# Optimization experiments

Measured on AMD Instinct MI355X. Metric: run time of the kernel, lower is better.

Reference implementation:

```python
import jax, jax.numpy as jnp
import numpy as np

N_HEAD = 16
N_KV_HEAD = 4
N_EMBD = 2048
HEAD_DIM = N_EMBD // N_HEAD
RMS_EPS = float(np.finfo(np.float32).eps)  # torch F.rms_norm default eps


def setup_inputs() -> dict:
    key = jax.random.key(0)
    ks = jax.random.split(key, 7)
    B, T = 2, 2048
    s = 0.02
    return {
        "x": jax.random.normal(ks[0], (B, T, N_EMBD), jnp.float32),
        "cos": jax.random.uniform(ks[1], (T, 1, HEAD_DIM), jnp.float32),
        "sin": jax.random.uniform(ks[2], (T, 1, HEAD_DIM), jnp.float32),
        "wq": jax.random.normal(ks[3], (N_HEAD * HEAD_DIM, N_EMBD), jnp.float32) * s,
        "wk": jax.random.normal(ks[4], (N_KV_HEAD * HEAD_DIM, N_EMBD), jnp.float32) * s,
        "wv": jax.random.normal(ks[5], (N_KV_HEAD * HEAD_DIM, N_EMBD), jnp.float32) * s,
        "wproj": jax.random.normal(ks[6], (N_EMBD, N_EMBD), jnp.float32) * s,
    }


def _rotate_half(x):
    h = x.shape[-1] // 2
    return jnp.concatenate([-x[..., h:], x[..., :h]], axis=-1)


def _apply_rope(x, cos, sin):  # x: [B, T, H, D]; cos/sin: [T, 1, D]
    return x * cos + _rotate_half(x) * sin


def _rms_norm(x):
    var = jnp.mean(jnp.square(x), axis=-1, keepdims=True)
    return x * jax.lax.rsqrt(var + RMS_EPS)


def reference(x, cos, sin, wq, wk, wv, wproj):
    B, T, C = x.shape
    group = N_HEAD // N_KV_HEAD
    q = (x @ wq.T).reshape(B, T, N_HEAD, HEAD_DIM)
    k = (x @ wk.T).reshape(B, T, N_KV_HEAD, HEAD_DIM)
    v = (x @ wv.T).reshape(B, T, N_KV_HEAD, HEAD_DIM)
    q = _rms_norm(_apply_rope(q, cos, sin))  # RoPE then QK RMSNorm
    k = _rms_norm(_apply_rope(k, cos, sin))
    # to [B, H, T, D]; expand kv heads for GQA
    q = q.transpose(0, 2, 1, 3)
    k = jnp.repeat(k.transpose(0, 2, 1, 3), group, axis=1)
    v = jnp.repeat(v.transpose(0, 2, 1, 3), group, axis=1)
    scale = 1.0 / jnp.sqrt(jnp.asarray(HEAD_DIM, x.dtype))
    scores = jnp.einsum('bhqd,bhkd->bhqk', q, k) * scale
    causal = jnp.tril(jnp.ones((T, T), bool))
    scores = jnp.where(causal, scores, jnp.asarray(-jnp.inf, scores.dtype))
    attn = jax.nn.softmax(scores, axis=-1)
    y = jnp.einsum('bhqk,bhkd->bhqd', attn, v)
    y = y.transpose(0, 2, 1, 3).reshape(B, T, C)
    return y @ wproj.T
```

## Files before the change

### kernel.cpp

```cpp
#include <hip/hip_runtime.h>
#include <hip/hip_bf16.h>

typedef __hip_bfloat16 bf16;
typedef __attribute__((ext_vector_type(8))) __bf16 bf16x8;
typedef __attribute__((ext_vector_type(4))) float f32x4;

#define MFMA16(a, b, c) __builtin_amdgcn_mfma_f32_16x16x32_bf16((a), (b), (c), 0, 0, 0)

#define BT 4096
#define CE 2048
#define NQKV 3072
#define TSEQ 2048
#define HD 128

#define QSCALE (0.08838834764831845f * 1.4426950408889634f)
#define M2 16.3222f

__device__ __forceinline__ void gld16(const void* g, void* l)
{
    __builtin_amdgcn_global_load_lds(
        (const __attribute__((address_space(1))) void*)g,
        (__attribute__((address_space(3))) void*)l, 16, 0, 0);
}

__global__ void detect_dtype(const unsigned short* __restrict__ x, int* __restrict__ flag)
{
    __shared__ int cnt;
    if (threadIdx.x == 0) cnt = 0;
    __syncthreads();
    unsigned short w = x[2 * threadIdx.x];
    int e = (w >> 7) & 0xFF;
    atomicAdd(&cnt, (e >= 117 && e <= 130) ? 1 : 0);
    __syncthreads();
    if (threadIdx.x == 0) *flag = (cnt < 128) ? 1 : 0;
}

__device__ __forceinline__ void stage8(short* dst, const void* src, size_t eoff, bool f32)
{
    if (f32) {
        const float* s = (const float*)src + eoff;
        float4 f0 = *(const float4*)s;
        float4 f1 = *(const float4*)(s + 4);
        bf16x8 v;
        v[0] = (__bf16)f0.x; v[1] = (__bf16)f0.y; v[2] = (__bf16)f0.z; v[3] = (__bf16)f0.w;
        v[4] = (__bf16)f1.x; v[5] = (__bf16)f1.y; v[6] = (__bf16)f1.z; v[7] = (__bf16)f1.w;
        *(bf16x8*)dst = v;
    } else {
        *(uint4*)dst = *(const uint4*)((const bf16*)src + eoff);
    }
}

__device__ __forceinline__ float ldf(const void* p, int i, bool f32)
{
    return f32 ? ((const float*)p)[i] : __bfloat162float(((const bf16*)p)[i]);
}

__global__ __launch_bounds__(256)
void conv_bf16(const void* __restrict__ src, bf16* __restrict__ dst,
               const int* __restrict__ flagp)
{
    const bool f = *flagp != 0;
    size_t i8 = (size_t)blockIdx.x * 256 + threadIdx.x;
    stage8((short*)(dst + i8 * 8), src, i8 * 8, f);
}

__global__ __launch_bounds__(256)
void gemm_bt(const void* __restrict__ A, const bf16* __restrict__ W,
             void* __restrict__ C, int M, int N, int K, int lda,
             int aGate, int oGate, const int* __restrict__ flagp)
{
    __shared__ short As[128][32];
    __shared__ short Bs[128][32];

    const int f = *flagp;
    const bool aF = aGate && f, oF = oGate && f;

    const int tid   = threadIdx.x;
    const int lane  = tid & 63;
    const int wid   = tid >> 6;
    const int row16 = lane & 15;
    const int quad  = lane >> 4;
    const int wr    = wid >> 1;
    const int wc    = wid & 1;
    const int m0    = blockIdx.y * 128;
    const int n0    = blockIdx.x * 128;

    const int rl4 = wid * 16 + (lane >> 2);
    const int c8  = (lane & 3) * 8;

    f32x4 acc[4][4];
#pragma unroll
    for (int i = 0; i < 4; i++)
#pragma unroll
        for (int j = 0; j < 4; j++)
            acc[i][j] = (f32x4){0.f, 0.f, 0.f, 0.f};

    for (int k0 = 0; k0 < K; k0 += 32) {
#pragma unroll
        for (int i = 0; i < 2; i++) {
            int r = i * 64 + rl4;
            gld16(W + (size_t)(n0 + r) * K + k0 + c8, &Bs[r][c8]);
        }
        if (!aF) {
#pragma unroll
            for (int i = 0; i < 2; i++) {
                int r = i * 64 + rl4;
                gld16((const bf16*)A + (size_t)(m0 + r) * lda + k0 + c8, &As[r][c8]);
            }
        } else {
#pragma unroll
            for (int i = 0; i < 2; i++) {
                int c = i * 256 + tid;
                int row = c >> 2, col = (c & 3) << 3;
                stage8(&As[row][col], A, (size_t)(m0 + row) * lda + k0 + col, true);
            }
        }
        __syncthreads();

        bf16x8 af[4], bfv[4];
#pragma unroll
        for (int mi = 0; mi < 4; mi++)
            af[mi] = *(const bf16x8*)&As[wr * 64 + mi * 16 + row16][quad * 8];
#pragma unroll
        for (int ni = 0; ni < 4; ni++)
            bfv[ni] = *(const bf16x8*)&Bs[wc * 64 + ni * 16 + row16][quad * 8];
#pragma unroll
        for (int mi = 0; mi < 4; mi++)
#pragma unroll
            for (int ni = 0; ni < 4; ni++)
                acc[mi][ni] = MFMA16(af[mi], bfv[ni], acc[mi][ni]);
        __syncthreads();
    }

#pragma unroll
    for (int mi = 0; mi < 4; mi++) {
        int rowb = m0 + wr * 64 + mi * 16 + quad * 4;
#pragma unroll
        for (int ni = 0; ni < 4; ni++) {
            int col = n0 + wc * 64 + ni * 16 + row16;
#pragma unroll
            for (int r = 0; r < 4; r++) {
                size_t idx = (size_t)(rowb + r) * N + col;
                float  v   = acc[mi][ni][r];
                if (oF) ((float*)C)[idx] = v;
                else    ((bf16*)C)[idx]  = __float2bfloat16(v);
            }
        }
    }
}

__global__ __launch_bounds__(256)
void rope_rms(bf16* __restrict__ qkv, const void* __restrict__ cosp,
              const void* __restrict__ sinp, const int* __restrict__ flagp)
{
    const bool f = *flagp != 0;
    const int wg   = blockIdx.x * 4 + (threadIdx.x >> 6);
    const int lane = threadIdx.x & 63;
    const int s    = wg % 20;
    const int m    = wg / 20;
    const int t    = m & (TSEQ - 1);

    const int col = (s < 16) ? s * HD : CE + (s - 16) * HD;
    bf16* p = qkv + (size_t)m * NQKV + col;

    float xlo = __bfloat162float(p[lane]);
    float xhi = __bfloat162float(p[lane + 64]);
    float cl  = ldf(cosp, t * HD + lane, f);
    float sl  = ldf(sinp, t * HD + lane, f);
    float ch  = ldf(cosp, t * HD + 64 + lane, f);
    float sh  = ldf(sinp, t * HD + 64 + lane, f);

    float rlo = xlo * cl - xhi * sl;
    float rhi = xhi * ch + xlo * sh;

    float ss = rlo * rlo + rhi * rhi;
#pragma unroll
    for (int off = 32; off > 0; off >>= 1)
        ss += __shfl_xor(ss, off, 64);
    float inv = rsqrtf(ss * (1.0f / 128.0f) + 1.1920929e-07f);
    if (s < 16) inv *= QSCALE;

    p[lane]      = __float2bfloat16(rlo * inv);
    p[lane + 64] = __float2bfloat16(rhi * inv);
}

__global__ __launch_bounds__(256)
void vtrans(const bf16* __restrict__ qkv, bf16* __restrict__ vt)
{
    int idx = blockIdx.x * 256 + threadIdx.x;
    int t  = idx & (TSEQ - 1);
    int d  = (idx >> 11) & 127;
    int bh = idx >> 18;
    vt[idx] = qkv[((size_t)((bh >> 2) * TSEQ + t)) * NQKV + 2560 + (bh & 3) * HD + d];
}

__global__ __launch_bounds__(512, 2)
void attn(bf16* __restrict__ qkv, const bf16* __restrict__ vt)
{
    __shared__ __bf16 Ks[2][64][128];
    __shared__ __bf16 Vs[2][128][64];
    __shared__ __bf16 Pl[8][2][16][72];

    const int tid   = threadIdx.x;
    const int lane  = tid & 63;
    const int wid   = tid >> 6;
    const int row16 = lane & 15;
    const int quad  = lane >> 4;
    const int b   = blockIdx.y >> 2;
    const int hk  = blockIdx.y & 3;
    const int h   = hk * 4 + (wid & 3);
    const int mh  = wid >> 2;
    const int xi  = blockIdx.x;
    const int q0  = xi * 64;
    const int qr0 = q0 + mh * 32;

    const bf16* Q  = qkv + ((size_t)(b * TSEQ + qr0)) * NQKV + h * HD;
    const bf16* Kp = qkv + ((size_t)(b * TSEQ)) * NQKV + CE + hk * HD;
    const bf16* Vp = vt + ((size_t)(b * 4 + hk) * HD) * TSEQ;

    char* const KsB = (char*)Ks;
    char* const VsB = (char*)Vs;

    auto stage = [&](int buf, int k0) {
#pragma unroll
        for (int i = 0; i < 2; i++) {
            int kr = (wid << 3) + i * 4 + (lane >> 4);
            int kc = (lane & 15) ^ (kr & 7);
            gld16(Kp + (size_t)(k0 + kr) * NQKV + kc * 8,
                  KsB + buf * 16384 + ((wid << 3) + i * 4) * 256 + lane * 16);
            int vr = (wid << 4) + i * 8 + (lane >> 3);
            int vc = (lane & 7) ^ (vr & 7);
            gld16(Vp + (size_t)vr * TSEQ + k0 + vc * 8,
                  VsB + buf * 16384 + ((wid << 4) + i * 8) * 128 + lane * 16);
        }
    };

    bf16x8 aq[2][4];
#pragma unroll
    for (int mi = 0; mi < 2; mi++)
#pragma unroll
        for (int ds = 0; ds < 4; ds++)
            aq[mi][ds] = *(const bf16x8*)(Q + (size_t)(mi * 16 + row16) * NQKV
                                          + ds * 32 + quad * 8);

    f32x4 o[2][8];
#pragma unroll
    for (int mi = 0; mi < 2; mi++)
#pragma unroll
        for (int dt = 0; dt < 8; dt++)
            o[mi][dt] = (f32x4){0.f, 0.f, 0.f, 0.f};
    float lsum[2][4] = {{0.f, 0.f, 0.f, 0.f}, {0.f, 0.f, 0.f, 0.f}};

    stage(0, 0);
    __syncthreads();

    for (int t = 0; t <= xi; t++) {
        const int cur = t & 1;
        if (t < xi) stage(cur ^ 1, (t + 1) * 64);

        f32x4 s[2][4];
#pragma unroll
        for (int mi = 0; mi < 2; mi++)
#pragma unroll
            for (int kg = 0; kg < 4; kg++)
                s[mi][kg] = (f32x4){0.f, 0.f, 0.f, 0.f};

        __builtin_amdgcn_s_setprio(1);
#pragma unroll
        for (int ds = 0; ds < 4; ds++) {
#pragma unroll
            for (int kg = 0; kg < 4; kg++) {
                int krow = kg * 16 + row16;
                int phys = (ds * 4 + quad) ^ (row16 & 7);
                bf16x8 kf = *(const bf16x8*)(KsB + cur * 16384 + krow * 256 + phys * 16);
                s[0][kg] = MFMA16(aq[0][ds], kf, s[0][kg]);
                s[1][kg] = MFMA16(aq[1][ds], kf, s[1][kg]);
            }
        }
        __builtin_amdgcn_s_setprio(0);

        const bool diag = (t == xi);
        const int  k0   = t * 64;
#pragma unroll
        for (int mi = 0; mi < 2; mi++) {
#pragma unroll
            for (int r = 0; r < 4; r++) {
                float p[4];
                int qrow = qr0 + mi * 16 + quad * 4 + r;
#pragma unroll
                for (int kg = 0; kg < 4; kg++) {
                    float e = __builtin_amdgcn_exp2f(s[mi][kg][r] - M2);
                    p[kg] = (!diag || (k0 + kg * 16 + row16 <= qrow)) ? e : 0.f;
                }
                lsum[mi][r] += (p[0] + p[1]) + (p[2] + p[3]);
#pragma unroll
                for (int kg = 0; kg < 4; kg++)
                    Pl[wid][mi][quad * 4 + r][kg * 16 + row16] = (__bf16)p[kg];
            }
        }
        __asm__ volatile("" ::: "memory");

        __builtin_amdgcn_s_setprio(1);
#pragma unroll
        for (int c = 0; c < 2; c++) {
            bf16x8 pf0 = *(const bf16x8*)&Pl[wid][0][row16][c * 32 + quad * 8];
            bf16x8 pf1 = *(const bf16x8*)&Pl[wid][1][row16][c * 32 + quad * 8];
#pragma unroll
            for (int dt = 0; dt < 8; dt++) {
                int vrow = dt * 16 + row16;
                int phys = (c * 4 + quad) ^ (row16 & 7);
                bf16x8 vf = *(const bf16x8*)(VsB + cur * 16384 + vrow * 128 + phys * 16);
                o[0][dt] = MFMA16(pf0, vf, o[0][dt]);
                o[1][dt] = MFMA16(pf1, vf, o[1][dt]);
            }
        }
        __builtin_amdgcn_s_setprio(0);
        __asm__ volatile("" ::: "memory");
        __syncthreads();
    }

#pragma unroll
    for (int mi = 0; mi < 2; mi++) {
#pragma unroll
        for (int r = 0; r < 4; r++) {
            float l = lsum[mi][r];
#pragma unroll
            for (int off = 1; off < 16; off <<= 1)
                l += __shfl_xor(l, off, 64);
            float rl = 1.0f / l;
            int trow = qr0 + mi * 16 + quad * 4 + r;
            bf16* dst = qkv + ((size_t)(b * TSEQ + trow)) * NQKV + h * HD;
#pragma unroll
            for (int dt = 0; dt < 8; dt++)
                dst[dt * 16 + row16] = __float2bfloat16(o[mi][dt][r] * rl);
        }
    }
}

extern "C" void kernel_launch(void* const* d_in, const int* in_sizes, int n_in,
                              void* d_out, int out_size, void* d_ws, size_t ws_size,
                              hipStream_t stream)
{
    bf16* qkv   = (bf16*)d_ws;
    bf16* vt    = qkv + (size_t)BT * NQKV;
    bf16* wqkvb = vt + (size_t)2 * 4 * HD * TSEQ;
    int* flagp  = (int*)(wqkvb + (size_t)NQKV * CE);

    detect_dtype<<<1, 256, 0, stream>>>((const unsigned short*)d_in[0], flagp);

    conv_bf16<<<(2048 * 2048 / 8) / 256, 256, 0, stream>>>(d_in[3], wqkvb, flagp);
    conv_bf16<<<(512 * 2048 / 8) / 256, 256, 0, stream>>>(d_in[4], wqkvb + (size_t)2048 * 2048, flagp);
    conv_bf16<<<(512 * 2048 / 8) / 256, 256, 0, stream>>>(d_in[5], wqkvb + (size_t)2560 * 2048, flagp);

    gemm_bt<<<dim3(NQKV / 128, BT / 128), 256, 0, stream>>>(
        d_in[0], wqkvb, qkv, BT, NQKV, CE, CE, 1, 0, flagp);

    conv_bf16<<<(2048 * 2048 / 8) / 256, 256, 0, stream>>>(d_in[6], wqkvb, flagp);

    vtrans<<<(2 * 4 * HD * TSEQ) / 256, 256, 0, stream>>>(qkv, vt);

    rope_rms<<<(BT * 20) / 4, 256, 0, stream>>>(qkv, d_in[1], d_in[2], flagp);

    attn<<<dim3(TSEQ / 64, 2 * 4), 512, 0, stream>>>(qkv, vt);

    gemm_bt<<<dim3(CE / 128, BT / 128), 256, 0, stream>>>(
        qkv, wqkvb, d_out, BT, CE, CE, NQKV, 0, 1, flagp);
}
```

Before: 369.1 us.

## Add 256x256 triple-buffered GEMM kernel for QKV and output projections

Adds a new 8-wave GEMM kernel with 256x256 tiles, a three-stage LDS ring fed by direct global-to-LDS loads, XOR swizzling and split MFMA phases with priority hints. The QKV projection now first converts x to bf16 in workspace (when the workspace is large enough) so the new kernel can read it, and the output projection always uses the new kernel. Larger tiles are meant to raise data reuse and overlap loads with MFMA work. The cost is an extra conversion pass over x, and the bigger tiles give only 128 or 192 workgroups, which may underfill the device's compute units.

```diff
diff --git a/kernel.cpp b/kernel.cpp
--- a/kernel.cpp
+++ b/kernel.cpp
@@ -135,6 +135,131 @@
 #pragma unroll
     for (int mi = 0; mi < 4; mi++) {
         int rowb = m0 + wr * 64 + mi * 16 + quad * 4;
+#pragma unroll
+        for (int ni = 0; ni < 4; ni++) {
+            int col = n0 + wc * 64 + ni * 16 + row16;
+#pragma unroll
+            for (int r = 0; r < 4; r++) {
+                size_t idx = (size_t)(rowb + r) * N + col;
+                float  v   = acc[mi][ni][r];
+                if (oF) ((float*)C)[idx] = v;
+                else    ((bf16*)C)[idx]  = __float2bfloat16(v);
+            }
+        }
+    }
+}
+
+__global__ __launch_bounds__(512, 2)
+void gemm8(const bf16* __restrict__ A, const bf16* __restrict__ W,
+           void* __restrict__ C, int M, int N, int K, int lda,
+           int oGate, const int* __restrict__ flagp)
+{
+    __shared__ __bf16 As[3][256][32];
+    __shared__ __bf16 Bs[3][256][32];
+
+    const bool oF = oGate && (*flagp != 0);
+
+    const int tid   = threadIdx.x;
+    const int lane  = tid & 63;
+    const int wid   = tid >> 6;
+    const int row16 = lane & 15;
+    const int quad  = lane >> 4;
+    const int wr    = wid >> 2;
+    const int wc    = wid & 3;
+    const int m0    = blockIdx.y * 256;
+    const int n0    = blockIdx.x * 256;
+    const int NT    = K >> 5;
+
+    const int srow = tid >> 2;
+    const int sc   = (tid & 3) ^ (srow & 3);
+    const bf16* Ag = A + (size_t)(m0 + srow) * lda + sc * 8;
+    const bf16* Bg = W + (size_t)(n0 + srow) * K   + sc * 8;
+    char* const AsB = (char*)As;
+    char* const BsB = (char*)Bs;
+    const int sdst = tid * 16;
+
+    auto stA = [&](int kt, int sb) {
+#pragma unroll
+        for (int u = 0; u < 2; ++u)
+            gld16(Ag + (size_t)(u * 128) * lda + kt * 32,
+                  AsB + sb + u * 8192 + sdst);
+    };
+    auto stB = [&](int kt, int sb) {
+#pragma unroll
+        for (int u = 0; u < 2; ++u)
+            gld16(Bg + (size_t)(u * 128) * K + kt * 32,
+                  BsB + sb + u * 8192 + sdst);
+    };
+
+    const int swzB  = (quad ^ (row16 & 3)) * 16;
+    const int raOff = (wr * 128 + row16) * 64 + swzB;
+    const int rbOff = (wc * 64  + row16) * 64 + swzB;
+
+    f32x4 acc[8][4];
+#pragma unroll
+    for (int i = 0; i < 8; i++)
+#pragma unroll
+        for (int j = 0; j < 4; j++)
+            acc[i][j] = (f32x4){0.f, 0.f, 0.f, 0.f};
+
+    stA(0, 0);     stB(0, 0);
+    stA(1, 16384); stB(1, 16384);
+    asm volatile("s_waitcnt vmcnt(4)" ::: "memory");
+    __builtin_amdgcn_s_barrier();
+    __builtin_amdgcn_sched_barrier(0);
+
+    int sl = 0, sl2 = 2;
+    for (int t = 0; t < NT; ++t) {
+        const int sb  = sl  * 16384;
+        const int sb2 = sl2 * 16384;
+        const bool pf = (t + 2) < NT;
+
+        bf16x8 af0[4], bfr[4];
+#pragma unroll
+        for (int ni = 0; ni < 4; ni++)
+            bfr[ni] = *(const bf16x8*)(BsB + sb + rbOff + ni * 1024);
+#pragma unroll
+        for (int mi = 0; mi < 4; mi++)
+            af0[mi] = *(const bf16x8*)(AsB + sb + raOff + mi * 1024);
+        if (pf) stA(t + 2, sb2);
+        __builtin_amdgcn_s_barrier();
+        asm volatile("s_waitcnt lgkmcnt(0)" ::: "memory");
+        __builtin_amdgcn_s_setprio(1);
+#pragma unroll
+        for (int mi = 0; mi < 4; mi++)
+#pragma unroll
+            for (int ni = 0; ni < 4; ni++)
+                acc[mi][ni] = MFMA16(af0[mi], bfr[ni], acc[mi][ni]);
+        __builtin_amdgcn_s_setprio(0);
+        __builtin_amdgcn_s_barrier();
+        __builtin_amdgcn_sched_barrier(0);
+
+        bf16x8 af1[4];
+#pragma unroll
+        for (int mi = 0; mi < 4; mi++)
+            af1[mi] = *(const bf16x8*)(AsB + sb + raOff + (4 + mi) * 1024);
+        if (pf) stB(t + 2, sb2);
+        if (t < NT - 2) asm volatile("s_waitcnt vmcnt(4)" ::: "memory");
+        else            asm volatile("s_waitcnt vmcnt(0)" ::: "memory");
+        __builtin_amdgcn_s_barrier();
+        asm volatile("s_waitcnt lgkmcnt(0)" ::: "memory");
+        __builtin_amdgcn_s_setprio(1);
+#pragma unroll
+        for (int mi = 0; mi < 4; mi++)
+#pragma unroll
+            for (int ni = 0; ni < 4; ni++)
+                acc[4 + mi][ni] = MFMA16(af1[mi], bfr[ni], acc[4 + mi][ni]);
+        __builtin_amdgcn_s_setprio(0);
+        __builtin_amdgcn_s_barrier();
+        __builtin_amdgcn_sched_barrier(0);
+
+        sl  = (sl  == 2) ? 0 : sl  + 1;
+        sl2 = (sl2 == 2) ? 0 : sl2 + 1;
+    }
+
+#pragma unroll
+    for (int mi = 0; mi < 8; mi++) {
+        int rowb = m0 + wr * 128 + mi * 16 + quad * 4;
 #pragma unroll
         for (int ni = 0; ni < 4; ni++) {
             int col = n0 + wc * 64 + ni * 16 + row16;
@@ -345,6 +470,11 @@
     bf16* vt    = qkv + (size_t)BT * NQKV;
     bf16* wqkvb = vt + (size_t)2 * 4 * HD * TSEQ;
     int* flagp  = (int*)(wqkvb + (size_t)NQKV * CE);
+    bf16* xb    = wqkvb + (size_t)NQKV * CE + 16;
+
+    const size_t need = ((size_t)BT * NQKV + (size_t)2 * 4 * HD * TSEQ
+                         + (size_t)NQKV * CE + 16 + (size_t)BT * CE) * sizeof(bf16);
+    const bool useXb = ws_size >= need;
 
     detect_dtype<<<1, 256, 0, stream>>>((const unsigned short*)d_in[0], flagp);
 
@@ -352,8 +482,14 @@
     conv_bf16<<<(512 * 2048 / 8) / 256, 256, 0, stream>>>(d_in[4], wqkvb + (size_t)2048 * 2048, flagp);
     conv_bf16<<<(512 * 2048 / 8) / 256, 256, 0, stream>>>(d_in[5], wqkvb + (size_t)2560 * 2048, flagp);
 
-    gemm_bt<<<dim3(NQKV / 128, BT / 128), 256, 0, stream>>>(
-        d_in[0], wqkvb, qkv, BT, NQKV, CE, CE, 1, 0, flagp);
+    if (useXb) {
+        conv_bf16<<<(BT * CE / 8) / 256, 256, 0, stream>>>(d_in[0], xb, flagp);
+        gemm8<<<dim3(NQKV / 256, BT / 256), 512, 0, stream>>>(
+            xb, wqkvb, qkv, BT, NQKV, CE, CE, 0, flagp);
+    } else {
+        gemm_bt<<<dim3(NQKV / 128, BT / 128), 256, 0, stream>>>(
+            d_in[0], wqkvb, qkv, BT, NQKV, CE, CE, 1, 0, flagp);
+    }
 
     conv_bf16<<<(2048 * 2048 / 8) / 256, 256, 0, stream>>>(d_in[6], wqkvb, flagp);
 
@@ -363,6 +499,6 @@
 
     attn<<<dim3(TSEQ / 64, 2 * 4), 512, 0, stream>>>(qkv, vt);
 
-    gemm_bt<<<dim3(CE / 128, BT / 128), 256, 0, stream>>>(
-        qkv, wqkvb, d_out, BT, CE, CE, NQKV, 0, 1, flagp);
-}
+    gemm8<<<dim3(CE / 256, BT / 256), 512, 0, stream>>>(
+        qkv, wqkvb, d_out, BT, CE, CE, NQKV, 1, flagp);
+}
```

Result: slower. 393.7 us (+6.7%).
